# Performance work log

Hardware: AMD Instinct MI355X
Metric: run time of the kernel (lower is better)

## Reference

```python
import jax, jax.numpy as jnp
import numpy as np

N, E = 50000, 800000
NF, HC, H, NC = 512, 64, 8, 16
NEG_SLOPE = 0.2


def setup_inputs() -> dict:
    key = jax.random.key(0)
    ks = jax.random.split(key, 10)
    x = jax.random.normal(ks[0], (N, NF), dtype=jnp.float32)
    edge_index = jax.random.randint(ks[1], (2, E), 0, N, dtype=jnp.int64)
    # layer 1 params (GATConv nf -> hc, heads=H, concat)
    w1 = jax.random.normal(ks[2], (NF, H * HC), dtype=jnp.float32) / np.sqrt(NF)
    a_src1 = jax.random.normal(ks[3], (H, HC), dtype=jnp.float32) / np.sqrt(HC)
    a_dst1 = jax.random.normal(ks[4], (H, HC), dtype=jnp.float32) / np.sqrt(HC)
    b1 = jnp.zeros((H * HC,), dtype=jnp.float32)
    # layer 2 params (GATConv hc*h -> nc, heads=1, concat=False)
    w2 = jax.random.normal(ks[5], (H * HC, NC), dtype=jnp.float32) / np.sqrt(H * HC)
    a_src2 = jax.random.normal(ks[6], (1, NC), dtype=jnp.float32) / np.sqrt(NC)
    a_dst2 = jax.random.normal(ks[7], (1, NC), dtype=jnp.float32) / np.sqrt(NC)
    b2 = jnp.zeros((NC,), dtype=jnp.float32)
    return {"x": x, "edge_index": edge_index, "w1": w1, "a_src1": a_src1,
            "a_dst1": a_dst1, "b1": b1, "w2": w2, "a_src2": a_src2,
            "a_dst2": a_dst2, "b2": b2}


def _gat_conv(x, src, dst, W, a_src, a_dst, heads, out_ch):
    # x: [N, F_in] -> h: [N, H, C]
    h = (x @ W).reshape(N, heads, out_ch)
    alpha_src = jnp.einsum('nhc,hc->nh', h, a_src)  # [N, H]
    alpha_dst = jnp.einsum('nhc,hc->nh', h, a_dst)  # [N, H]
    e = jax.nn.leaky_relu(alpha_src[src] + alpha_dst[dst], NEG_SLOPE)  # [E', H]
    # segment-wise softmax over edges grouped by destination node
    m = jax.ops.segment_max(e, dst, num_segments=N)
    ex = jnp.exp(e - m[dst])
    denom = jax.ops.segment_sum(ex, dst, num_segments=N)
    alpha = ex / denom[dst]  # [E', H]
    out = jax.ops.segment_sum(h[src] * alpha[:, :, None], dst, num_segments=N)
    return out  # [N, H, C]


def reference(x, edge_index, w1, a_src1, a_dst1, b1, w2, a_src2, a_dst2, b2):
    # add self loops (PyG GATConv default)
    loops = jnp.arange(N, dtype=edge_index.dtype)
    src = jnp.concatenate([edge_index[0], loops])
    dst = jnp.concatenate([edge_index[1], loops])
    # layer 1: heads concatenated, dropout is identity in eval mode
    emb = _gat_conv(x, src, dst, w1, a_src1, a_dst1, H, HC).reshape(N, H * HC) + b1
    h_act = jax.nn.elu(emb)
    # layer 2: single head, no concat
    logits = _gat_conv(h_act, src, dst, w2, a_src2, a_dst2, 1, NC).reshape(N, NC) + b2
    return (logits, emb)
```

## Files before the change

kernel.cpp:

```cpp
#include <hip/hip_runtime.h>
#include <math.h>

#define N_NODES 50000
#define M_PAD   50048
#define N_EDGES 800000
#define ET (N_EDGES + N_NODES)
#define NF 512
#define HC 64
#define NH 8
#define D1 512
#define NC 16
#define NEG_SLOPE 0.2f

typedef __attribute__((ext_vector_type(8))) short bf16x8;
typedef __attribute__((ext_vector_type(4))) float floatx4;

static __device__ __forceinline__ float b2f(unsigned short u) {
  union { unsigned int i; float f; } v; v.i = ((unsigned int)u) << 16; return v.f;
}
static __device__ __forceinline__ unsigned short f2b(float f) {
  union { float f; unsigned int i; } v; v.f = f;
  unsigned int r = v.i + 0x7fffu + ((v.i >> 16) & 1u);
  return (unsigned short)(r >> 16);
}

static __device__ __forceinline__ void async_cp16(const void* g, void* l) {
  __builtin_amdgcn_global_load_lds(
      (const __attribute__((address_space(1))) unsigned int*)g,
      (__attribute__((address_space(3))) unsigned int*)l, 16, 0, 0);
}

__global__ __launch_bounds__(256) void k_wdeg(const float* __restrict__ w1,
                                              unsigned short* __restrict__ w1t,
                                              const int* __restrict__ ei,
                                              int* __restrict__ deg) {
  const int b = blockIdx.x;
  if (b < 256) {
    __shared__ float t[32][33];
    int tx = threadIdx.x & 31, ty = threadIdx.x >> 5;
    int k0 = (b & 15) * 32, n0 = (b >> 4) * 32;
    for (int r = ty; r < 32; r += 8)
      t[r][tx] = w1[(size_t)(k0 + r) * D1 + n0 + tx];
    __syncthreads();
    for (int r = ty; r < 32; r += 8)
      w1t[(size_t)(n0 + r) * NF + k0 + tx] = f2b(t[tx][r]);
  }
  int i = b * 256 + threadIdx.x;
  if (i < ET) {
    int dst = (i < N_EDGES) ? ei[N_EDGES + i] : (i - N_EDGES);
    atomicAdd(&deg[dst], 1);
  }
}

__global__ __launch_bounds__(512) void k_gemm1f(const float* __restrict__ x,
                                                const unsigned short* __restrict__ w1t,
                                                unsigned short* __restrict__ h1b,
                                                const float* __restrict__ a_src1,
                                                const float* __restrict__ a_dst1,
                                                float* __restrict__ as1,
                                                float* __restrict__ ad1) {
  __shared__ unsigned short As[128 * 32];
  __shared__ unsigned short Bs[2][512 * 32];
  const int tid  = threadIdx.x;
  const int w    = tid >> 6;
  const int lane = tid & 63;
  const int l16  = lane & 15;
  const int quad = lane >> 4;
  const int bm   = blockIdx.x * 128;
  const int wr   = (w >> 1) * 32;
  const int half = w & 1;
  const int wc   = half * 256;

  const int arow = tid >> 2;
  const int acg  = tid & 3;
  const int aswz = (acg ^ ((arow >> 1) & 3)) * 8;
  const bool aval = (bm + arow) < N_NODES;
  const float* agp = x + (size_t)(bm + arow) * NF + acg * 8;

  const int bn_base = w * 16 + (lane >> 2);
  const int bkd = (lane & 3) * 8;
  const int bks = ((lane & 3) ^ ((lane >> 3) & 3)) * 8;

  const int rswz = (quad ^ ((l16 >> 1) & 3)) * 8;

  floatx4 acc[2][16] = {};
  floatx4 ar0 = {0.f, 0.f, 0.f, 0.f}, ar1 = {0.f, 0.f, 0.f, 0.f};

#pragma unroll
  for (int r = 0; r < 4; ++r) {
    const int n = r * 128 + bn_base;
    async_cp16(w1t + (size_t)n * NF + bks, &Bs[0][n * 32 + bkd]);
  }
  if (aval) {
    ar0 = __builtin_nontemporal_load((const floatx4*)agp);
    ar1 = __builtin_nontemporal_load((const floatx4*)(agp + 4));
  }

  for (int s = 0; s < NF / 32; ++s) {
    const int cur = s & 1;
    bf16x8 av;
    av[0] = (short)f2b(ar0[0]); av[1] = (short)f2b(ar0[1]);
    av[2] = (short)f2b(ar0[2]); av[3] = (short)f2b(ar0[3]);
    av[4] = (short)f2b(ar1[0]); av[5] = (short)f2b(ar1[1]);
    av[6] = (short)f2b(ar1[2]); av[7] = (short)f2b(ar1[3]);
    *(bf16x8*)&As[arow * 32 + aswz] = av;
    __syncthreads();

    if (s + 1 < NF / 32) {
      const int kk1 = (s + 1) * 32;
#pragma unroll
      for (int r = 0; r < 4; ++r) {
        const int n = r * 128 + bn_base;
        async_cp16(w1t + (size_t)n * NF + kk1 + bks, &Bs[cur ^ 1][n * 32 + bkd]);
      }
      if (aval) {
        ar0 = __builtin_nontemporal_load((const floatx4*)(agp + kk1));
        ar1 = __builtin_nontemporal_load((const floatx4*)(agp + kk1 + 4));
      }
    }

    bf16x8 af0 = *(const bf16x8*)&As[(wr + l16) * 32 + rswz];
    bf16x8 af1 = *(const bf16x8*)&As[(wr + 16 + l16) * 32 + rswz];
#pragma unroll
    for (int j = 0; j < 16; ++j) {
      bf16x8 bf = *(const bf16x8*)&Bs[cur][(wc + j * 16 + l16) * 32 + rswz];
      acc[0][j] = __builtin_amdgcn_mfma_f32_16x16x32_bf16(af0, bf, acc[0][j], 0, 0, 0);
      acc[1][j] = __builtin_amdgcn_mfma_f32_16x16x32_bf16(af1, bf, acc[1][j], 0, 0, 0);
    }
    __syncthreads();
  }

#pragma unroll
  for (int i = 0; i < 2; ++i)
#pragma unroll
    for (int j = 0; j < 16; ++j) {
      const int col = wc + j * 16 + l16;
#pragma unroll
      for (int r = 0; r < 4; ++r) {
        const int row = bm + wr + i * 16 + quad * 4 + r;
        h1b[(size_t)row * D1 + col] = f2b(acc[i][j][r]);
      }
    }

  float* alpS = (float*)&Bs[0][0];
  float* alpD = alpS + 128 * 9;
  float afs[16], ads[16];
#pragma unroll
  for (int j = 0; j < 16; ++j) {
    afs[j] = a_src1[wc + j * 16 + l16];
    ads[j] = a_dst1[wc + j * 16 + l16];
  }
#pragma unroll
  for (int i = 0; i < 2; ++i)
#pragma unroll
    for (int r = 0; r < 4; ++r) {
      float s0 = 0.f, s1 = 0.f, s2 = 0.f, s3 = 0.f;
      float d0 = 0.f, d1 = 0.f, d2 = 0.f, d3 = 0.f;
#pragma unroll
      for (int j = 0; j < 16; ++j) {
        float v = acc[i][j][r];
        if ((j >> 2) == 0) { s0 += v * afs[j]; d0 += v * ads[j]; }
        if ((j >> 2) == 1) { s1 += v * afs[j]; d1 += v * ads[j]; }
        if ((j >> 2) == 2) { s2 += v * afs[j]; d2 += v * ads[j]; }
        if ((j >> 2) == 3) { s3 += v * afs[j]; d3 += v * ads[j]; }
      }
#pragma unroll
      for (int m = 1; m < 16; m <<= 1) {
        s0 += __shfl_xor(s0, m); s1 += __shfl_xor(s1, m);
        s2 += __shfl_xor(s2, m); s3 += __shfl_xor(s3, m);
        d0 += __shfl_xor(d0, m); d1 += __shfl_xor(d1, m);
        d2 += __shfl_xor(d2, m); d3 += __shfl_xor(d3, m);
      }
      if (l16 == 0) {
        const int rl = wr + i * 16 + quad * 4 + r;
        alpS[rl * 9 + half * 4 + 0] = s0; alpS[rl * 9 + half * 4 + 1] = s1;
        alpS[rl * 9 + half * 4 + 2] = s2; alpS[rl * 9 + half * 4 + 3] = s3;
        alpD[rl * 9 + half * 4 + 0] = d0; alpD[rl * 9 + half * 4 + 1] = d1;
        alpD[rl * 9 + half * 4 + 2] = d2; alpD[rl * 9 + half * 4 + 3] = d3;
      }
    }
  __syncthreads();
#pragma unroll
  for (int e = 0; e < 2; ++e) {
    const int idx = tid + e * 512;
    const int rl = idx >> 3, hd = idx & 7;
    const int n = bm + rl;
    if (n < N_NODES) {
      as1[n * NH + hd] = alpS[rl * 9 + hd];
      ad1[n * NH + hd] = alpD[rl * 9 + hd];
    }
  }
}

__global__ void k_reduce(const int* __restrict__ deg, int* __restrict__ bsums) {
  __shared__ int s[1024];
  int i = blockIdx.x * 1024 + threadIdx.x;
  s[threadIdx.x] = (i < N_NODES) ? deg[i] : 0;
  __syncthreads();
  for (int off = 512; off > 0; off >>= 1) {
    if (threadIdx.x < off) s[threadIdx.x] += s[threadIdx.x + off];
    __syncthreads();
  }
  if (threadIdx.x == 0) bsums[blockIdx.x] = s[0];
}

__global__ __launch_bounds__(1024) void k_scan_final(const int* __restrict__ deg,
                                                     const int* __restrict__ bsums,
                                                     int* __restrict__ rowp,
                                                     int* __restrict__ pos) {
  __shared__ int ws[16];
  __shared__ int sprefix;
  const int tid = threadIdx.x, bid = blockIdx.x;
  const int lane = tid & 63, wid = tid >> 6;

  if (tid < 64) {
    int v = (tid < 49) ? bsums[tid] : 0;
    int inc = v;
#pragma unroll
    for (int off = 1; off < 64; off <<= 1) {
      int u = __shfl_up(inc, off);
      if (tid >= off) inc += u;
    }
    if (tid == bid) sprefix = inc - v;
  }

  const int i = bid * 1024 + tid;
  int v = (i < N_NODES) ? deg[i] : 0;
  int inc = v;
#pragma unroll
  for (int off = 1; off < 64; off <<= 1) {
    int u = __shfl_up(inc, off);
    if (lane >= off) inc += u;
  }
  if (lane == 63) ws[wid] = inc;
  __syncthreads();
  if (tid < 16) {
    int wv = ws[tid];
    int winc = wv;
#pragma unroll
    for (int off = 1; off < 16; off <<= 1) {
      int u = __shfl_up(winc, off);
      if (tid >= off) winc += u;
    }
    ws[tid] = winc - wv;
  }
  __syncthreads();
  const int ex = inc - v + ws[wid] + sprefix;
  if (i < N_NODES) { rowp[i] = ex; pos[i] = ex; }
  if (i == N_NODES - 1) rowp[N_NODES] = ex + v;
}

__global__ void k_scatter(const int* __restrict__ ei, int* __restrict__ pos,
                          int* __restrict__ csr) {
  int i = blockIdx.x * 256 + threadIdx.x;
  if (i >= ET) return;
  int s, d;
  if (i < N_EDGES) { s = ei[i]; d = ei[N_EDGES + i]; }
  else             { s = d = i - N_EDGES; }
  int slot = atomicAdd(&pos[d], 1);
  csr[slot] = s;
}

static __device__ __forceinline__ void ld_edge1(const unsigned short* __restrict__ h1b,
                                                const float* __restrict__ as1,
                                                int src, int head, int col,
                                                bf16x8& hv, float& al) {
  al = as1[src * NH + head];
  hv = *(const bf16x8*)&h1b[(size_t)src * D1 + col];
}

static __device__ __forceinline__ void use_edge1(const bf16x8& hv, float al, float adv,
                                                 float& den, float acc[8]) {
  float e = al + adv;
  e = (e >= 0.f) ? e : NEG_SLOPE * e;
  float wgt = __expf(e);
  den += wgt;
#pragma unroll
  for (int jj = 0; jj < 8; ++jj) acc[jj] += wgt * b2f((unsigned short)hv[jj]);
}

__global__ __launch_bounds__(256) void k_agg1(const unsigned short* __restrict__ h1b,
                                              const float* __restrict__ as1,
                                              const float* __restrict__ ad1,
                                              const int* __restrict__ rowp,
                                              const int* __restrict__ csr,
                                              const float* __restrict__ b1,
                                              float* __restrict__ emb) {
  const int wid  = threadIdx.x >> 6;
  const int lane = threadIdx.x & 63;
  const int node = blockIdx.x * 4 + wid;
  if (node >= N_NODES) return;
  const int start = rowp[node], end = rowp[node + 1];
  const int head = lane >> 3;
  const int col  = lane * 8;
  const float adv = ad1[node * NH + head];

  bf16x8 h0, h1, h2, h3;
  float  a0, a1, a2, a3;

  {
    int i0 = __builtin_nontemporal_load(&csr[start]);
    int i1 = (start + 1 < end) ? __builtin_nontemporal_load(&csr[start + 1]) : 0;
    int i2 = (start + 2 < end) ? __builtin_nontemporal_load(&csr[start + 2]) : 0;
    int i3 = (start + 3 < end) ? __builtin_nontemporal_load(&csr[start + 3]) : 0;
    ld_edge1(h1b, as1, i0, head, col, h0, a0);
    if (start + 1 < end) ld_edge1(h1b, as1, i1, head, col, h1, a1);
    if (start + 2 < end) ld_edge1(h1b, as1, i2, head, col, h2, a2);
    if (start + 3 < end) ld_edge1(h1b, as1, i3, head, col, h3, a3);
  }

  float den = 0.f;
  float acc[8] = {};
  for (int j = start; j < end; j += 4) {
    int n0 = (j + 4 < end) ? __builtin_nontemporal_load(&csr[j + 4]) : 0;
    int n1 = (j + 5 < end) ? __builtin_nontemporal_load(&csr[j + 5]) : 0;
    int n2 = (j + 6 < end) ? __builtin_nontemporal_load(&csr[j + 6]) : 0;
    int n3 = (j + 7 < end) ? __builtin_nontemporal_load(&csr[j + 7]) : 0;
    use_edge1(h0, a0, adv, den, acc);
    if (j + 4 < end) ld_edge1(h1b, as1, n0, head, col, h0, a0);
    if (j + 1 < end) use_edge1(h1, a1, adv, den, acc);
    if (j + 5 < end) ld_edge1(h1b, as1, n1, head, col, h1, a1);
    if (j + 2 < end) use_edge1(h2, a2, adv, den, acc);
    if (j + 6 < end) ld_edge1(h1b, as1, n2, head, col, h2, a2);
    if (j + 3 < end) use_edge1(h3, a3, adv, den, acc);
    if (j + 7 < end) ld_edge1(h1b, as1, n3, head, col, h3, a3);
  }
  const float rden = 1.f / den;

  const float4 bb0 = *(const float4*)&b1[col];
  const float4 bb1 = *(const float4*)&b1[col + 4];
  float4 o0 = make_float4(acc[0] * rden + bb0.x, acc[1] * rden + bb0.y,
                          acc[2] * rden + bb0.z, acc[3] * rden + bb0.w);
  float4 o1 = make_float4(acc[4] * rden + bb1.x, acc[5] * rden + bb1.y,
                          acc[6] * rden + bb1.z, acc[7] * rden + bb1.w);
  *(float4*)&emb[(size_t)node * D1 + col]     = o0;
  *(float4*)&emb[(size_t)node * D1 + col + 4] = o1;
}

static __device__ __forceinline__ void split_bf16(float x, unsigned short& h,
                                                  unsigned short& l) {
  h = f2b(x);
  float rem = x - b2f(h);
  l = f2b(rem);
}

__global__ __launch_bounds__(256) void k_gemm2m(const float* __restrict__ emb,
                                                const float* __restrict__ W2,
                                                const float* __restrict__ a_src2,
                                                const float* __restrict__ a_dst2,
                                                float* __restrict__ h2,
                                                float* __restrict__ as2,
                                                float* __restrict__ ad2) {
  const int wv   = threadIdx.x >> 6;
  const int lane = threadIdx.x & 63;
  const int l16  = lane & 15;
  const int quad = lane >> 4;
  const int n0 = blockIdx.x * 128 + wv * 32 + l16;
  const int n1 = n0 + 16;
  const bool v0 = n0 < N_NODES, v1 = n1 < N_NODES;

  floatx4 acc0 = {0.f, 0.f, 0.f, 0.f};
  floatx4 acc1 = {0.f, 0.f, 0.f, 0.f};

  const float* e0 = emb + (size_t)n0 * D1 + quad * 8;
  const float* e1 = emb + (size_t)n1 * D1 + quad * 8;
  const float* wp = W2 + (size_t)(quad * 8) * NC + l16;

#pragma unroll 2
  for (int kk = 0; kk < D1; kk += 32) {
    bf16x8 ah, al;
#pragma unroll
    for (int j = 0; j < 8; ++j) {
      float wv2 = wp[(size_t)(kk + j) * NC];
      unsigned short h, l;
      split_bf16(wv2, h, l);
      ah[j] = (short)h; al[j] = (short)l;
    }
    bf16x8 bh0, bl0, bh1, bl1;
    {
      floatx4 pa = {0.f, 0.f, 0.f, 0.f}, pb = {0.f, 0.f, 0.f, 0.f};
      if (v0) {
        pa = *(const floatx4*)&e0[kk];
        pb = *(const floatx4*)&e0[kk + 4];
      }
      float t[8] = {pa[0], pa[1], pa[2], pa[3], pb[0], pb[1], pb[2], pb[3]};
#pragma unroll
      for (int j = 0; j < 8; ++j) {
        float xx = t[j];
        float s = (xx > 0.f) ? xx : (__expf(xx) - 1.f);
        unsigned short h, l;
        split_bf16(s, h, l);
        bh0[j] = (short)h; bl0[j] = (short)l;
      }
    }
    {
      floatx4 pa = {0.f, 0.f, 0.f, 0.f}, pb = {0.f, 0.f, 0.f, 0.f};
      if (v1) {
        pa = *(const floatx4*)&e1[kk];
        pb = *(const floatx4*)&e1[kk + 4];
      }
      float t[8] = {pa[0], pa[1], pa[2], pa[3], pb[0], pb[1], pb[2], pb[3]};
#pragma unroll
      for (int j = 0; j < 8; ++j) {
        float xx = t[j];
        float s = (xx > 0.f) ? xx : (__expf(xx) - 1.f);
        unsigned short h, l;
        split_bf16(s, h, l);
        bh1[j] = (short)h; bl1[j] = (short)l;
      }
    }
    acc0 = __builtin_amdgcn_mfma_f32_16x16x32_bf16(ah, bh0, acc0, 0, 0, 0);
    acc0 = __builtin_amdgcn_mfma_f32_16x16x32_bf16(ah, bl0, acc0, 0, 0, 0);
    acc0 = __builtin_amdgcn_mfma_f32_16x16x32_bf16(al, bh0, acc0, 0, 0, 0);
    acc1 = __builtin_amdgcn_mfma_f32_16x16x32_bf16(ah, bh1, acc1, 0, 0, 0);
    acc1 = __builtin_amdgcn_mfma_f32_16x16x32_bf16(ah, bl1, acc1, 0, 0, 0);
    acc1 = __builtin_amdgcn_mfma_f32_16x16x32_bf16(al, bh1, acc1, 0, 0, 0);
  }

  const float4 asv = ((const float4*)a_src2)[quad];
  const float4 adv = ((const float4*)a_dst2)[quad];
  float sa0 = acc0[0] * asv.x + acc0[1] * asv.y + acc0[2] * asv.z + acc0[3] * asv.w;
  float da0 = acc0[0] * adv.x + acc0[1] * adv.y + acc0[2] * adv.z + acc0[3] * adv.w;
  float sa1 = acc1[0] * asv.x + acc1[1] * asv.y + acc1[2] * asv.z + acc1[3] * asv.w;
  float da1 = acc1[0] * adv.x + acc1[1] * adv.y + acc1[2] * adv.z + acc1[3] * adv.w;
  sa0 += __shfl_xor(sa0, 16); sa0 += __shfl_xor(sa0, 32);
  da0 += __shfl_xor(da0, 16); da0 += __shfl_xor(da0, 32);
  sa1 += __shfl_xor(sa1, 16); sa1 += __shfl_xor(sa1, 32);
  da1 += __shfl_xor(da1, 16); da1 += __shfl_xor(da1, 32);

  if (v0) {
    *(float4*)&h2[(size_t)n0 * NC + quad * 4] =
        make_float4(acc0[0], acc0[1], acc0[2], acc0[3]);
    if (quad == 0) { as2[n0] = sa0; ad2[n0] = da0; }
  }
  if (v1) {
    *(float4*)&h2[(size_t)n1 * NC + quad * 4] =
        make_float4(acc1[0], acc1[1], acc1[2], acc1[3]);
    if (quad == 0) { as2[n1] = sa1; ad2[n1] = da1; }
  }
}

__global__ __launch_bounds__(256) void k_agg2(const float* __restrict__ h2,
                                              const float* __restrict__ as2,
                                              const float* __restrict__ ad2,
                                              const int* __restrict__ rowp,
                                              const int* __restrict__ csr,
                                              const float* __restrict__ b2,
                                              float* __restrict__ logits) {
  const int wid  = threadIdx.x >> 6;
  const int lane = threadIdx.x & 63;
  const int node = blockIdx.x * 4 + wid;
  if (node >= N_NODES) return;
  const int start = rowp[node], end = rowp[node + 1];
  const float adv = ad2[node];
  const int g = lane >> 4;
  const int c = lane & 15;

  int jA = start + g;
  int sA = (jA < end) ? csr[jA] : -1;
  int jB = jA + 4;
  int sB = (jB < end) ? csr[jB] : -1;
  float eA = 0.f, vA = 0.f;
  if (sA >= 0) { eA = as2[sA]; vA = h2[(size_t)sA * NC + c]; }

  float den = 0.f, acc = 0.f;
  for (int base = start; base < end; base += 4) {
    float eB = 0.f, vB = 0.f;
    if (sB >= 0) { eB = as2[sB]; vB = h2[(size_t)sB * NC + c]; }
    int jC = base + 8 + g;
    int sC = (jC < end) ? csr[jC] : -1;
    if (sA >= 0) {
      float e = eA + adv;
      e = (e >= 0.f) ? e : NEG_SLOPE * e;
      float wgt = __expf(e);
      den += wgt;
      acc += wgt * vA;
    }
    sA = sB; eA = eB; vA = vB; sB = sC;
  }
  acc += __shfl_xor(acc, 16); acc += __shfl_xor(acc, 32);
  den += __shfl_xor(den, 16); den += __shfl_xor(den, 32);
  if (lane < 16) logits[(size_t)node * NC + lane] = acc / den + b2[lane];
}

extern "C" void kernel_launch(void* const* d_in, const int* in_sizes, int n_in,
                              void* d_out, int out_size, void* d_ws, size_t ws_size,
                              hipStream_t stream) {
  const float* x      = (const float*)d_in[0];
  const int*   ei     = (const int*)d_in[1];
  const float* w1     = (const float*)d_in[2];
  const float* a_src1 = (const float*)d_in[3];
  const float* a_dst1 = (const float*)d_in[4];
  const float* b1     = (const float*)d_in[5];
  const float* w2     = (const float*)d_in[6];
  const float* a_src2 = (const float*)d_in[7];
  const float* a_dst2 = (const float*)d_in[8];
  const float* b2     = (const float*)d_in[9];

  char* w = (char*)d_ws;
  char* xb_region = w;
  w += (size_t)M_PAD * NF * 2;
  unsigned short* h1b = (unsigned short*)w; w += (size_t)M_PAD * D1 * 2;
  unsigned short* w1t = (unsigned short*)w; w += (size_t)NF * D1 * 2;
  float* as1 = (float*)w;  w += (size_t)N_NODES * NH * 4;
  float* ad1 = (float*)w;  w += (size_t)N_NODES * NH * 4;
  int* deg   = (int*)w;    w += (size_t)N_NODES * 4;
  int* rowp  = (int*)w;    w += (size_t)50064 * 4;
  int* pos   = (int*)w;    w += (size_t)N_NODES * 4;
  int* csr   = (int*)w;    w += (size_t)ET * 4;
  int* bsums = (int*)w;    w += 256;
  float* h2  = (float*)xb_region;
  float* as2 = (float*)(xb_region + (size_t)N_NODES * NC * 4);
  float* ad2 = (float*)(xb_region + (size_t)N_NODES * NC * 4 + (size_t)N_NODES * 4);

  float* logits = (float*)d_out;
  float* emb    = (float*)d_out + (size_t)N_NODES * NC;

  hipMemsetAsync(deg, 0, N_NODES * sizeof(int), stream);

  k_wdeg<<<(ET + 255) / 256, 256, 0, stream>>>(w1, w1t, ei, deg);
  k_gemm1f<<<M_PAD / 128, 512, 0, stream>>>(x, w1t, h1b, a_src1, a_dst1, as1, ad1);

  k_reduce<<<49, 1024, 0, stream>>>(deg, bsums);
  k_scan_final<<<49, 1024, 0, stream>>>(deg, bsums, rowp, pos);
  k_scatter<<<(ET + 255) / 256, 256, 0, stream>>>(ei, pos, csr);

  k_agg1<<<(N_NODES + 3) / 4, 256, 0, stream>>>(h1b, as1, ad1, rowp, csr, b1, emb);

  k_gemm2m<<<(N_NODES + 127) / 128, 256, 0, stream>>>(emb, w2, a_src2, a_dst2, h2, as2, ad2);
  k_agg2<<<(N_NODES + 3) / 4, 256, 0, stream>>>(h2, as2, ad2, rowp, csr, b2, logits);
}
```

Measured before the change: 518.3 us.

## Split GEMM1 output columns across two blocks to halve per-block tile

The first-layer GEMM now launches a 2D grid in which each block computes a 128x256 tile instead of 128x512, so each wave holds half as many accumulators and the B shared-memory buffer is halved. This lowers register and LDS pressure and doubles the block count, aiming for better occupancy and latency hiding. The cost is that each x row tile is read and converted to bf16 twice. The nontemporal loads of x become ordinary loads, presumably so the second block can hit in cache. The attention logits are now produced four heads per block.

```diff
diff --git a/kernel.cpp b/kernel.cpp
--- a/kernel.cpp
+++ b/kernel.cpp
@@ -60,16 +60,18 @@
                                                 float* __restrict__ as1,
                                                 float* __restrict__ ad1) {
   __shared__ unsigned short As[128 * 32];
-  __shared__ unsigned short Bs[2][512 * 32];
+  __shared__ unsigned short Bs[2][256 * 32];
   const int tid  = threadIdx.x;
   const int w    = tid >> 6;
   const int lane = tid & 63;
   const int l16  = lane & 15;
   const int quad = lane >> 4;
-  const int bm   = blockIdx.x * 128;
+  const int bx   = blockIdx.x;
+  const int bc   = bx * 256;
+  const int bm   = blockIdx.y * 128;
   const int wr   = (w >> 1) * 32;
   const int half = w & 1;
-  const int wc   = half * 256;
+  const int wc   = half * 128;
 
   const int arow = tid >> 2;
   const int acg  = tid & 3;
@@ -83,17 +85,17 @@
 
   const int rswz = (quad ^ ((l16 >> 1) & 3)) * 8;
 
-  floatx4 acc[2][16] = {};
+  floatx4 acc[2][8] = {};
   floatx4 ar0 = {0.f, 0.f, 0.f, 0.f}, ar1 = {0.f, 0.f, 0.f, 0.f};
 
 #pragma unroll
-  for (int r = 0; r < 4; ++r) {
+  for (int r = 0; r < 2; ++r) {
     const int n = r * 128 + bn_base;
-    async_cp16(w1t + (size_t)n * NF + bks, &Bs[0][n * 32 + bkd]);
+    async_cp16(w1t + (size_t)(bc + n) * NF + bks, &Bs[0][n * 32 + bkd]);
   }
   if (aval) {
-    ar0 = __builtin_nontemporal_load((const floatx4*)agp);
-    ar1 = __builtin_nontemporal_load((const floatx4*)(agp + 4));
+    ar0 = *(const floatx4*)agp;
+    ar1 = *(const floatx4*)(agp + 4);
   }
 
   for (int s = 0; s < NF / 32; ++s) {
@@ -109,20 +111,20 @@
     if (s + 1 < NF / 32) {
       const int kk1 = (s + 1) * 32;
 #pragma unroll
-      for (int r = 0; r < 4; ++r) {
+      for (int r = 0; r < 2; ++r) {
         const int n = r * 128 + bn_base;
-        async_cp16(w1t + (size_t)n * NF + kk1 + bks, &Bs[cur ^ 1][n * 32 + bkd]);
+        async_cp16(w1t + (size_t)(bc + n) * NF + kk1 + bks, &Bs[cur ^ 1][n * 32 + bkd]);
       }
       if (aval) {
-        ar0 = __builtin_nontemporal_load((const floatx4*)(agp + kk1));
-        ar1 = __builtin_nontemporal_load((const floatx4*)(agp + kk1 + 4));
+        ar0 = *(const floatx4*)(agp + kk1);
+        ar1 = *(const floatx4*)(agp + kk1 + 4);
       }
     }
 
     bf16x8 af0 = *(const bf16x8*)&As[(wr + l16) * 32 + rswz];
     bf16x8 af1 = *(const bf16x8*)&As[(wr + 16 + l16) * 32 + rswz];
 #pragma unroll
-    for (int j = 0; j < 16; ++j) {
+    for (int j = 0; j < 8; ++j) {
       bf16x8 bf = *(const bf16x8*)&Bs[cur][(wc + j * 16 + l16) * 32 + rswz];
       acc[0][j] = __builtin_amdgcn_mfma_f32_16x16x32_bf16(af0, bf, acc[0][j], 0, 0, 0);
       acc[1][j] = __builtin_amdgcn_mfma_f32_16x16x32_bf16(af1, bf, acc[1][j], 0, 0, 0);
@@ -133,8 +135,8 @@
 #pragma unroll
   for (int i = 0; i < 2; ++i)
 #pragma unroll
-    for (int j = 0; j < 16; ++j) {
-      const int col = wc + j * 16 + l16;
+    for (int j = 0; j < 8; ++j) {
+      const int col = bc + wc + j * 16 + l16;
 #pragma unroll
       for (int r = 0; r < 4; ++r) {
         const int row = bm + wr + i * 16 + quad * 4 + r;
@@ -143,51 +145,43 @@
     }
 
   float* alpS = (float*)&Bs[0][0];
-  float* alpD = alpS + 128 * 9;
-  float afs[16], ads[16];
-#pragma unroll
-  for (int j = 0; j < 16; ++j) {
-    afs[j] = a_src1[wc + j * 16 + l16];
-    ads[j] = a_dst1[wc + j * 16 + l16];
+  float* alpD = alpS + 128 * 5;
+  float afs[8], ads[8];
+#pragma unroll
+  for (int j = 0; j < 8; ++j) {
+    afs[j] = a_src1[bc + wc + j * 16 + l16];
+    ads[j] = a_dst1[bc + wc + j * 16 + l16];
   }
 #pragma unroll
   for (int i = 0; i < 2; ++i)
 #pragma unroll
     for (int r = 0; r < 4; ++r) {
-      float s0 = 0.f, s1 = 0.f, s2 = 0.f, s3 = 0.f;
-      float d0 = 0.f, d1 = 0.f, d2 = 0.f, d3 = 0.f;
-#pragma unroll
-      for (int j = 0; j < 16; ++j) {
+      float s0 = 0.f, s1 = 0.f, d0 = 0.f, d1 = 0.f;
+#pragma unroll
+      for (int j = 0; j < 8; ++j) {
         float v = acc[i][j][r];
         if ((j >> 2) == 0) { s0 += v * afs[j]; d0 += v * ads[j]; }
-        if ((j >> 2) == 1) { s1 += v * afs[j]; d1 += v * ads[j]; }
-        if ((j >> 2) == 2) { s2 += v * afs[j]; d2 += v * ads[j]; }
-        if ((j >> 2) == 3) { s3 += v * afs[j]; d3 += v * ads[j]; }
+        else               { s1 += v * afs[j]; d1 += v * ads[j]; }
       }
 #pragma unroll
       for (int m = 1; m < 16; m <<= 1) {
         s0 += __shfl_xor(s0, m); s1 += __shfl_xor(s1, m);
-        s2 += __shfl_xor(s2, m); s3 += __shfl_xor(s3, m);
         d0 += __shfl_xor(d0, m); d1 += __shfl_xor(d1, m);
-        d2 += __shfl_xor(d2, m); d3 += __shfl_xor(d3, m);
       }
       if (l16 == 0) {
         const int rl = wr + i * 16 + quad * 4 + r;
-        alpS[rl * 9 + half * 4 + 0] = s0; alpS[rl * 9 + half * 4 + 1] = s1;
-        alpS[rl * 9 + half * 4 + 2] = s2; alpS[rl * 9 + half * 4 + 3] = s3;
-        alpD[rl * 9 + half * 4 + 0] = d0; alpD[rl * 9 + half * 4 + 1] = d1;
-        alpD[rl * 9 + half * 4 + 2] = d2; alpD[rl * 9 + half * 4 + 3] = d3;
+        const int hl = half * 2;
+        alpS[rl * 5 + hl]     = s0; alpS[rl * 5 + hl + 1] = s1;
+        alpD[rl * 5 + hl]     = d0; alpD[rl * 5 + hl + 1] = d1;
       }
     }
   __syncthreads();
-#pragma unroll
-  for (int e = 0; e < 2; ++e) {
-    const int idx = tid + e * 512;
-    const int rl = idx >> 3, hd = idx & 7;
+  {
+    const int rl = tid >> 2, hd = tid & 3;
     const int n = bm + rl;
     if (n < N_NODES) {
-      as1[n * NH + hd] = alpS[rl * 9 + hd];
-      ad1[n * NH + hd] = alpD[rl * 9 + hd];
+      as1[n * NH + bx * 4 + hd] = alpS[rl * 5 + hd];
+      ad1[n * NH + bx * 4 + hd] = alpD[rl * 5 + hd];
     }
   }
 }
@@ -519,7 +513,7 @@
   hipMemsetAsync(deg, 0, N_NODES * sizeof(int), stream);
 
   k_wdeg<<<(ET + 255) / 256, 256, 0, stream>>>(w1, w1t, ei, deg);
-  k_gemm1f<<<M_PAD / 128, 512, 0, stream>>>(x, w1t, h1b, a_src1, a_dst1, as1, ad1);
+  k_gemm1f<<<dim3(2, M_PAD / 128), 512, 0, stream>>>(x, w1t, h1b, a_src1, a_dst1, as1, ad1);
 
   k_reduce<<<49, 1024, 0, stream>>>(deg, bsums);
   k_scan_final<<<49, 1024, 0, stream>>>(deg, bsums, rowp, pos);
```

New measurement: 536.0 us. +3.4%, slower.
